# Kernel optimization log

Measured on AMD Instinct MI355X. Metric: run time of the kernel, lower is better.

The kernel has to match this reference:

```python
import jax, jax.numpy as jnp
import numpy as np

FS = 24000.0
C_SOUND = 343.0
MAX_TAU = 6
IGNORE = -100
PAIRS = np.array([(0, 1), (0, 2), (0, 3), (1, 2), (1, 3), (2, 3)])  # m1<m2 loop order
PERMS_NP = np.array([(0, 1, 2), (0, 2, 1), (1, 0, 2), (1, 2, 0), (2, 0, 1), (2, 1, 0)])  # itertools order


def _mic_locs():
    # [rad, azi_deg, ele_deg] per mic, centered at origin (matches center_mic_coords)
    coords = np.array([[0.042, 45, 35], [0.042, -45, -35], [0.042, 135, -35], [0.042, -135, 35]], dtype=np.float64)
    rad = coords[:, 0]
    azi = coords[:, 1] * 2 * np.pi / 360
    ele = coords[:, 2] * 2 * np.pi / 360
    locs = np.stack([rad * np.cos(azi) * np.cos(ele), rad * np.sin(azi) * np.cos(ele), rad * np.sin(ele)], axis=1)
    return jnp.asarray(locs, dtype=jnp.float32)

MIC_LOCS = _mic_locs()  # [4,3]


def _get_tdoa_targets(target):
    """Vectorized get_tdoa_target. target: [B,T,E,5,C].
    Assumes <=1 active class per (b,t,track) so the random class shuffle is a no-op.
    Returns (tdoas, tdoas2) as int32 [B,T,E,6]."""
    B, T, E, F, C = target.shape
    active = target[:, :, :, 0, :]                                  # [B,T,E,C] 0/1 flags
    is_active = jnp.any(active > 0, axis=-1)                        # [B,T,E]
    doa = jnp.einsum('btec,btedc->bted', active, target[:, :, :, 1:4, :])  # [B,T,E,3]
    dist = jnp.einsum('btec,btec->bte', active, target[:, :, :, 4, :])     # [B,T,E]
    src = doa * dist[..., None]                                     # [B,T,E,3]
    d = jnp.linalg.norm(src[..., None, :] - MIC_LOCS, axis=-1)      # [B,T,E,4] dist to each mic
    tdoa = d[..., PAIRS[:, 0]] - d[..., PAIRS[:, 1]]                # [B,T,E,6]
    tdoa = jnp.round(tdoa * FS / C_SOUND) + MAX_TAU                 # [B,T,E,6]
    # compact active tracks to the front (stable keeps track order, matching tr_cnt)
    order = jnp.argsort(jnp.logical_not(is_active), axis=-1)        # [B,T,E]
    gathered = jnp.take_along_axis(tdoa, order[..., None], axis=2)  # [B,T,E,6]
    n = jnp.sum(is_active, axis=-1)                                 # [B,T] number of events
    k = jnp.arange(E)[None, None, :]                                # slot index
    idx1 = jnp.clip(jnp.minimum(k, n[:, :, None] - 1), 0, E - 1)    # pad with LAST event
    idx2 = jnp.where(k < n[:, :, None], k, 0)                       # pad with FIRST event
    tdoas = jnp.take_along_axis(gathered, idx1[..., None], axis=2)
    tdoas2 = jnp.take_along_axis(gathered, idx2[..., None], axis=2)
    empty = (n == 0)[:, :, None, None]
    tdoas = jnp.where(empty, float(IGNORE), tdoas)
    tdoas2 = jnp.where(empty, float(IGNORE), tdoas2)
    return tdoas.astype(jnp.int32), tdoas2.astype(jnp.int32)


def _forward(pred, t_a, t_b):
    B, T, C, Tr, ntd = pred.shape
    N = B * T * ntd
    p = pred.transpose(0, 1, 4, 2, 3).reshape(N, C, Tr)             # [N,C,Tr]
    ta = t_a.transpose(0, 1, 3, 2).reshape(N, Tr)                   # [N,Tr]
    tb = t_b.transpose(0, 1, 3, 2).reshape(N, Tr)
    logp = jax.nn.log_softmax(p, axis=1)                            # [N,C,Tr]
    perms = jnp.asarray(PERMS_NP)                                   # [6,Tr]
    ar = jnp.arange(Tr)

    def pit(t):
        tc = jnp.clip(t, 0, C - 1)
        # L[n,i,j] = CE(pred track j, target track i); ignore_index -> 0
        L = -jnp.take_along_axis(logp, jnp.broadcast_to(tc[:, :, None], (N, Tr, Tr)), axis=1)
        L = jnp.where((t == IGNORE)[:, :, None], 0.0, L)
        pl = L[:, ar[None, :], perms].mean(axis=-1)                 # [N,6] per-perm mean loss
        pidx = jnp.argmin(pl, axis=1)                               # first min (matches torch loop)
        return jnp.take_along_axis(pl, pidx[:, None], axis=1)[:, 0], perms[pidx]

    loss1, perm1 = pit(ta)
    loss2, perm2 = pit(tb)
    use2 = loss2 < loss1                                            # torch.min keeps first on ties
    loss = jnp.where(use2, loss2, loss1)
    t_sel = jnp.where(use2[:, None], tb, ta)
    perm_sel = jnp.where(use2[:, None], perm2, perm1)

    pred_cls = jnp.argmax(p, axis=1)                                # [N,Tr]
    t_perm = jnp.take_along_axis(t_sel, perm_sel, axis=1)           # target reordered by opt perm
    valid = t_perm != IGNORE
    npred = jnp.sum(valid)
    correct = jnp.sum((pred_cls == t_perm) & valid)
    acc = jnp.where(npred > 0, correct.astype(jnp.float32) / jnp.maximum(npred, 1).astype(jnp.float32), 0.0)

    mask = loss > 0.0
    nval = jnp.sum(mask)
    lmean = jnp.where(nval > 0, jnp.sum(jnp.where(mask, loss, 0.0)) / jnp.maximum(nval, 1).astype(loss.dtype), 0.0)
    return lmean, acc


def setup_inputs() -> dict:
    key = jax.random.key(0)
    B, T, E, NCLS, NTD, CPRED = 128, 600, 3, 13, 6, 13
    k1, k2, k3, k4, k5 = jax.random.split(key, 5)
    pred = jax.random.normal(k1, (B, T, CPRED, E, NTD), dtype=jnp.float32)
    act_cls = jax.random.randint(k2, (B, T, E), 0, NCLS)
    act_flag = (jax.random.uniform(k3, (B, T, E)) < 0.5).astype(jnp.float32)
    onehot = jax.nn.one_hot(act_cls, NCLS, dtype=jnp.float32) * act_flag[..., None]  # <=1 active class/track
    doa = jax.random.normal(k4, (B, T, E, 3), dtype=jnp.float32)
    doa = doa / jnp.linalg.norm(doa, axis=-1, keepdims=True)
    dist = jax.random.uniform(k5, (B, T, E), minval=1.0, maxval=3.0, dtype=jnp.float32)
    target = jnp.concatenate([
        onehot[:, :, :, None, :],
        jnp.broadcast_to(doa[..., None], (B, T, E, 3, NCLS)),
        jnp.broadcast_to(dist[..., None, None], (B, T, E, 1, NCLS)),
    ], axis=3).astype(jnp.float32)                                  # [B,T,E,5,NCLS]
    return {"pred": pred, "target": target}


def reference(pred, target):
    t_a, t_b = _get_tdoa_targets(target)
    return _forward(pred, t_a, t_b)
```

## Files before the change

### kernel.cpp

```cpp
#include <hip/hip_runtime.h>
#include <cstdint>
#include <cstddef>

#define BT_TOTAL 76800
#define NCLS 13
#define IGN  (-100)

#define CPB   32
#define NBLK  (BT_TOTAL / CPB)
#define ITEMS (CPB * 6)
#define NF4T  (CPB * 195 / 4)
#define KT    7
#define NF4P  (CPB * 234 / 4)
#define KP    8

struct Partial { float ls; int lc; int cor; int val; };

__device__ __forceinline__ void stage16(const float4* __restrict__ g, float4* l) {
    __builtin_amdgcn_global_load_lds((const __attribute__((address_space(1))) void*)g,
                                     (__attribute__((address_space(3))) void*)l,
                                     16, 0, 0);
}

extern "C" __global__ __launch_bounds__(256)
void tdoa_fused(const float* __restrict__ pred, const float* __restrict__ target,
                Partial* __restrict__ part) {
    const int tid = threadIdx.x;
    const int cb  = blockIdx.x * CPB;

    __shared__ float4 sBuf4[NF4P];
    __shared__ uint32_t sTd[CPB * 12];
    const float* sBuf = (const float*)sBuf4;

    {
        const float4* gt = (const float4*)(target + (size_t)cb * 195);
#pragma unroll
        for (int k = 0; k < KT; k++) {
            const int i = k * 256 + tid;
            if (i < NF4T) stage16(gt + i, &sBuf4[i]);
        }
    }
    __syncthreads();

    if (tid < CPB) {
        const float* tg = sBuf + tid * 195;

        const float MX[4] = { 0.02432757455f,  0.02432757455f, -0.02432757455f, -0.02432757455f };
        const float MY[4] = { 0.02432757455f, -0.02432757455f,  0.02432757455f, -0.02432757455f };
        const float MZ[4] = { 0.02409021033f, -0.02409021033f, -0.02409021033f,  0.02409021033f };
        const int PI_[6] = {0,0,0,1,1,2};
        const int PJ_[6] = {1,2,3,2,3,3};

        int  td[3][6];
        bool ab[3];
        int  nact = 0;
#pragma unroll
        for (int e = 0; e < 3; e++) {
            float a[NCLS];
#pragma unroll
            for (int c = 0; c < NCLS; c++) a[c] = tg[e * 65 + c];
            bool ia = false;
#pragma unroll
            for (int c = 0; c < NCLS; c++) ia = ia || (a[c] > 0.0f);
            float d0 = 0.f, d1 = 0.f, d2 = 0.f, ds = 0.f;
#pragma unroll
            for (int c = 0; c < NCLS; c++) {
                d0 += a[c] * tg[e * 65 + 13 + c];
                d1 += a[c] * tg[e * 65 + 26 + c];
                d2 += a[c] * tg[e * 65 + 39 + c];
                ds += a[c] * tg[e * 65 + 52 + c];
            }
            const float sx = d0 * ds, sy = d1 * ds, sz = d2 * ds;
            float dm[4];
#pragma unroll
            for (int m = 0; m < 4; m++) {
                const float ex = sx - MX[m], ey = sy - MY[m], ez = sz - MZ[m];
                dm[m] = sqrtf(ex * ex + ey * ey + ez * ez);
            }
#pragma unroll
            for (int p = 0; p < 6; p++) {
                const float diff = dm[PI_[p]] - dm[PJ_[p]];
                td[e][p] = (int)rintf((diff * 24000.0f) / 343.0f) + 6;
            }
            ab[e] = ia;
            nact += ia ? 1 : 0;
        }

        const int o0 = ab[0] ? 0 : (ab[1] ? 1 : 2);
        const int o1 = (ab[0] && ab[1]) ? 1 : 2;
        const bool empty = (nact == 0);

#pragma unroll
        for (int p = 0; p < 6; p++) {
            const int g0 = (o0 == 0) ? td[0][p] : ((o0 == 1) ? td[1][p] : td[2][p]);
            const int g1 = (o1 == 1) ? td[1][p] : td[2][p];
            const int g2 = td[2][p];
            int ta0 = g0;
            int ta1 = (nact >= 2) ? g1 : g0;
            int ta2 = (nact == 3) ? g2 : ((nact == 2) ? g1 : g0);
            int tb0 = g0;
            int tb1 = (nact >= 2) ? g1 : g0;
            int tb2 = (nact == 3) ? g2 : g0;
            uint32_t w0 = (uint32_t)(ta0 & 0xff) | ((uint32_t)(ta1 & 0xff) << 8) | ((uint32_t)(ta2 & 0xff) << 16);
            uint32_t w1 = (uint32_t)(tb0 & 0xff) | ((uint32_t)(tb1 & 0xff) << 8) | ((uint32_t)(tb2 & 0xff) << 16);
            if (empty) { w0 = 0x009c9c9cu; w1 = 0x009c9c9cu; }
            sTd[tid * 12 + p * 2 + 0] = w0;
            sTd[tid * 12 + p * 2 + 1] = w1;
        }
    }
    __syncthreads();

    {
        const float4* gp = (const float4*)(pred + (size_t)cb * 234);
#pragma unroll
        for (int k = 0; k < KP; k++) {
            const int i = k * 256 + tid;
            if (i < NF4P) stage16(gp + i, &sBuf4[i]);
        }
    }
    __syncthreads();

    float lsum = 0.f;
    int   lcnt = 0, cor = 0, nval = 0;

    if (tid < ITEMS) {
        const int btl = tid / 6;
        const int p   = tid - btl * 6;
        const float* pp = sBuf + btl * 234 + p;

        float x[NCLS][3];
#pragma unroll
        for (int c = 0; c < NCLS; c++)
#pragma unroll
            for (int j = 0; j < 3; j++)
                x[c][j] = pp[c * 18 + j * 6];

        int   am[3];
        float lse[3];
#pragma unroll
        for (int j = 0; j < 3; j++) {
            float m = x[0][j]; int a = 0;
#pragma unroll
            for (int c = 1; c < NCLS; c++) { if (x[c][j] > m) { m = x[c][j]; a = c; } }
            float s = 0.f;
#pragma unroll
            for (int c = 0; c < NCLS; c++) s += expf(x[c][j] - m);
            am[j] = a; lse[j] = m + logf(s);
        }

        const uint32_t w0 = sTd[btl * 12 + p * 2 + 0];
        const uint32_t w1 = sTd[btl * 12 + p * 2 + 1];
        int ta[3], tb[3];
#pragma unroll
        for (int i = 0; i < 3; i++) {
            ta[i] = (int)(int8_t)(w0 >> (8 * i));
            tb[i] = (int)(int8_t)(w1 >> (8 * i));
        }

        float La[3][3], Lb[3][3];
#pragma unroll
        for (int i = 0; i < 3; i++) {
            const int  ca  = (ta[i] < 0) ? 0 : ta[i];
            const int  cb2 = (tb[i] < 0) ? 0 : tb[i];
            const bool ia  = (ta[i] == IGN);
            const bool ib  = (tb[i] == IGN);
#pragma unroll
            for (int j = 0; j < 3; j++) {
                La[i][j] = ia ? 0.f : (lse[j] - pp[ca  * 18 + j * 6]);
                Lb[i][j] = ib ? 0.f : (lse[j] - pp[cb2 * 18 + j * 6]);
            }
        }

        const int P0[6] = {0,0,1,1,2,2};
        const int P1[6] = {1,2,0,2,0,1};
        const int P2[6] = {2,1,2,0,1,0};
        float l1 = 0.f, l2 = 0.f; int i1 = 0, i2 = 0;
#pragma unroll
        for (int q = 0; q < 6; q++) {
            const float va = (La[0][P0[q]] + La[1][P1[q]] + La[2][P2[q]]) * (1.0f / 3.0f);
            const float vb = (Lb[0][P0[q]] + Lb[1][P1[q]] + Lb[2][P2[q]]) * (1.0f / 3.0f);
            if (q == 0) { l1 = va; l2 = vb; }
            else {
                if (va < l1) { l1 = va; i1 = q; }
                if (vb < l2) { l2 = vb; i2 = q; }
            }
        }

        const bool use2 = (l2 < l1);
        const float loss = use2 ? l2 : l1;
        const int  qsel = use2 ? i2 : i1;
        const int PK[6] = {36, 24, 33, 9, 18, 6};
        int pk = PK[0];
#pragma unroll
        for (int k = 1; k < 6; k++) pk = (qsel == k) ? PK[k] : pk;
        const int s0 = use2 ? tb[0] : ta[0];
        const int s1 = use2 ? tb[1] : ta[1];
        const int s2 = use2 ? tb[2] : ta[2];
#pragma unroll
        for (int i = 0; i < 3; i++) {
            const int pi = (pk >> (2 * i)) & 3;
            const int tp = (pi == 0) ? s0 : ((pi == 1) ? s1 : s2);
            const bool v = (tp != IGN);
            nval += v ? 1 : 0;
            cor  += (v && (am[i] == tp)) ? 1 : 0;
        }
        if (loss > 0.f) { lsum += loss; lcnt++; }
    }

#pragma unroll
    for (int off = 32; off > 0; off >>= 1) {
        lsum += __shfl_down(lsum, off, 64);
        lcnt += __shfl_down(lcnt, off, 64);
        cor  += __shfl_down(cor,  off, 64);
        nval += __shfl_down(nval, off, 64);
    }
    __shared__ float rf[4];
    __shared__ int   r1[4], r2[4], r3[4];
    const int wid = tid >> 6;
    if ((tid & 63) == 0) { rf[wid] = lsum; r1[wid] = lcnt; r2[wid] = cor; r3[wid] = nval; }
    __syncthreads();
    if (tid == 0) {
        Partial pt;
        pt.ls  = rf[0] + rf[1] + rf[2] + rf[3];
        pt.lc  = r1[0] + r1[1] + r1[2] + r1[3];
        pt.cor = r2[0] + r2[1] + r2[2] + r2[3];
        pt.val = r3[0] + r3[1] + r3[2] + r3[3];
        part[blockIdx.x] = pt;
    }
}

extern "C" __global__ __launch_bounds__(256)
void tdoa_final(const Partial* __restrict__ part, float* __restrict__ out) {
    const int tid = threadIdx.x;
    double ls = 0.0; int lc = 0, cor = 0, val = 0;
    for (int i = tid; i < NBLK; i += 256) {
        const Partial p = part[i];
        ls += (double)p.ls; lc += p.lc; cor += p.cor; val += p.val;
    }
#pragma unroll
    for (int off = 32; off > 0; off >>= 1) {
        ls  += __shfl_down(ls,  off, 64);
        lc  += __shfl_down(lc,  off, 64);
        cor += __shfl_down(cor, off, 64);
        val += __shfl_down(val, off, 64);
    }
    __shared__ double sd[4];
    __shared__ int    s1[4], s2[4], s3[4];
    const int wid = tid >> 6;
    if ((tid & 63) == 0) { sd[wid] = ls; s1[wid] = lc; s2[wid] = cor; s3[wid] = val; }
    __syncthreads();
    if (tid == 0) {
        const double L = sd[0] + sd[1] + sd[2] + sd[3];
        const int c1 = s1[0] + s1[1] + s1[2] + s1[3];
        const int c2 = s2[0] + s2[1] + s2[2] + s2[3];
        const int c3 = s3[0] + s3[1] + s3[2] + s3[3];
        out[0] = (c1 > 0) ? (float)(L / (double)c1) : 0.0f;
        out[1] = (c3 > 0) ? ((float)c2 / (float)c3) : 0.0f;
    }
}

extern "C" void kernel_launch(void* const* d_in, const int* in_sizes, int n_in,
                              void* d_out, int out_size, void* d_ws, size_t ws_size,
                              hipStream_t stream) {
    const float* pred   = (const float*)d_in[0];
    const float* target = (const float*)d_in[1];
    Partial* part = (Partial*)d_ws;
    float* out = (float*)d_out;
    hipLaunchKernelGGL(tdoa_fused, dim3(NBLK), dim3(256), 0, stream, pred, target, part);
    hipLaunchKernelGGL(tdoa_final, dim3(1),    dim3(256), 0, stream, part, out);
}
```

Baseline: 152.8 us.

## Parallelize TDOA target prologue across threads and overlap pred staging

The per-cell target decoding moves from 32 serial threads, each handling all three events and all six pairs, to one thread per (cell, event) for the mic distances and one thread per (cell, pair) for packing the TDOA words. Intermediate distances and activity flags pass through new shared arrays. The pred async load into LDS is now issued before the pair-packing phase, so it overlaps that compute and drops one barrier. Cells per block fall from 32 to 24 and threads per block from 256 to 192 (three waves), giving more, smaller blocks. The cost is an extra barrier and shared-memory round trip for the intermediates.

```diff
diff --git a/kernel.cpp b/kernel.cpp
--- a/kernel.cpp
+++ b/kernel.cpp
@@ -6,7 +6,8 @@
 #define NCLS 13
 #define IGN  (-100)
 
-#define CPB   32
+#define CPB   24
+#define BLKT  192
 #define NBLK  (BT_TOTAL / CPB)
 #define ITEMS (CPB * 6)
 #define NF4T  (CPB * 195 / 4)
@@ -22,7 +23,7 @@
                                      16, 0, 0);
 }
 
-extern "C" __global__ __launch_bounds__(256)
+extern "C" __global__ __launch_bounds__(BLKT)
 void tdoa_fused(const float* __restrict__ pred, const float* __restrict__ target,
                 Partial* __restrict__ part) {
     const int tid = threadIdx.x;
@@ -30,93 +31,97 @@
 
     __shared__ float4 sBuf4[NF4P];
     __shared__ uint32_t sTd[CPB * 12];
+    __shared__ float  dmS[CPB * 12];
+    __shared__ int    actS[CPB * 3];
     const float* sBuf = (const float*)sBuf4;
 
     {
         const float4* gt = (const float4*)(target + (size_t)cb * 195);
 #pragma unroll
         for (int k = 0; k < KT; k++) {
-            const int i = k * 256 + tid;
+            const int i = k * BLKT + tid;
             if (i < NF4T) stage16(gt + i, &sBuf4[i]);
         }
     }
     __syncthreads();
 
-    if (tid < CPB) {
-        const float* tg = sBuf + tid * 195;
+    if (tid < CPB * 3) {
+        const int cell = tid / 3;
+        const int e    = tid - cell * 3;
+        const float* tg = sBuf + cell * 195 + e * 65;
 
         const float MX[4] = { 0.02432757455f,  0.02432757455f, -0.02432757455f, -0.02432757455f };
         const float MY[4] = { 0.02432757455f, -0.02432757455f,  0.02432757455f, -0.02432757455f };
         const float MZ[4] = { 0.02409021033f, -0.02409021033f, -0.02409021033f,  0.02409021033f };
+
+        float a[NCLS];
+#pragma unroll
+        for (int c = 0; c < NCLS; c++) a[c] = tg[c];
+        bool ia = false;
+#pragma unroll
+        for (int c = 0; c < NCLS; c++) ia = ia || (a[c] > 0.0f);
+        float d0 = 0.f, d1 = 0.f, d2 = 0.f, ds = 0.f;
+#pragma unroll
+        for (int c = 0; c < NCLS; c++) {
+            d0 += a[c] * tg[13 + c];
+            d1 += a[c] * tg[26 + c];
+            d2 += a[c] * tg[39 + c];
+            ds += a[c] * tg[52 + c];
+        }
+        const float sx = d0 * ds, sy = d1 * ds, sz = d2 * ds;
+#pragma unroll
+        for (int m = 0; m < 4; m++) {
+            const float ex = sx - MX[m], ey = sy - MY[m], ez = sz - MZ[m];
+            dmS[cell * 12 + e * 4 + m] = sqrtf(ex * ex + ey * ey + ez * ez);
+        }
+        actS[cell * 3 + e] = ia ? 1 : 0;
+    }
+    __syncthreads();
+
+    {
+        const float4* gp = (const float4*)(pred + (size_t)cb * 234);
+#pragma unroll
+        for (int k = 0; k < KP; k++) {
+            const int i = k * BLKT + tid;
+            if (i < NF4P) stage16(gp + i, &sBuf4[i]);
+        }
+    }
+
+    if (tid < ITEMS) {
+        const int cell = tid / 6;
+        const int p    = tid - cell * 6;
         const int PI_[6] = {0,0,0,1,1,2};
         const int PJ_[6] = {1,2,3,2,3,3};
-
-        int  td[3][6];
-        bool ab[3];
-        int  nact = 0;
+        const int mi = PI_[p], mj = PJ_[p];
+
+        int td[3];
 #pragma unroll
         for (int e = 0; e < 3; e++) {
-            float a[NCLS];
-#pragma unroll
-            for (int c = 0; c < NCLS; c++) a[c] = tg[e * 65 + c];
-            bool ia = false;
-#pragma unroll
-            for (int c = 0; c < NCLS; c++) ia = ia || (a[c] > 0.0f);
-            float d0 = 0.f, d1 = 0.f, d2 = 0.f, ds = 0.f;
-#pragma unroll
-            for (int c = 0; c < NCLS; c++) {
-                d0 += a[c] * tg[e * 65 + 13 + c];
-                d1 += a[c] * tg[e * 65 + 26 + c];
-                d2 += a[c] * tg[e * 65 + 39 + c];
-                ds += a[c] * tg[e * 65 + 52 + c];
-            }
-            const float sx = d0 * ds, sy = d1 * ds, sz = d2 * ds;
-            float dm[4];
-#pragma unroll
-            for (int m = 0; m < 4; m++) {
-                const float ex = sx - MX[m], ey = sy - MY[m], ez = sz - MZ[m];
-                dm[m] = sqrtf(ex * ex + ey * ey + ez * ez);
-            }
-#pragma unroll
-            for (int p = 0; p < 6; p++) {
-                const float diff = dm[PI_[p]] - dm[PJ_[p]];
-                td[e][p] = (int)rintf((diff * 24000.0f) / 343.0f) + 6;
-            }
-            ab[e] = ia;
-            nact += ia ? 1 : 0;
-        }
-
-        const int o0 = ab[0] ? 0 : (ab[1] ? 1 : 2);
-        const int o1 = (ab[0] && ab[1]) ? 1 : 2;
-        const bool empty = (nact == 0);
-
-#pragma unroll
-        for (int p = 0; p < 6; p++) {
-            const int g0 = (o0 == 0) ? td[0][p] : ((o0 == 1) ? td[1][p] : td[2][p]);
-            const int g1 = (o1 == 1) ? td[1][p] : td[2][p];
-            const int g2 = td[2][p];
-            int ta0 = g0;
-            int ta1 = (nact >= 2) ? g1 : g0;
-            int ta2 = (nact == 3) ? g2 : ((nact == 2) ? g1 : g0);
-            int tb0 = g0;
-            int tb1 = (nact >= 2) ? g1 : g0;
-            int tb2 = (nact == 3) ? g2 : g0;
-            uint32_t w0 = (uint32_t)(ta0 & 0xff) | ((uint32_t)(ta1 & 0xff) << 8) | ((uint32_t)(ta2 & 0xff) << 16);
-            uint32_t w1 = (uint32_t)(tb0 & 0xff) | ((uint32_t)(tb1 & 0xff) << 8) | ((uint32_t)(tb2 & 0xff) << 16);
-            if (empty) { w0 = 0x009c9c9cu; w1 = 0x009c9c9cu; }
-            sTd[tid * 12 + p * 2 + 0] = w0;
-            sTd[tid * 12 + p * 2 + 1] = w1;
-        }
-    }
-    __syncthreads();
-
-    {
-        const float4* gp = (const float4*)(pred + (size_t)cb * 234);
-#pragma unroll
-        for (int k = 0; k < KP; k++) {
-            const int i = k * 256 + tid;
-            if (i < NF4P) stage16(gp + i, &sBuf4[i]);
-        }
+            const float diff = dmS[cell * 12 + e * 4 + mi] - dmS[cell * 12 + e * 4 + mj];
+            td[e] = (int)rintf((diff * 24000.0f) / 343.0f) + 6;
+        }
+        const bool ab0 = actS[cell * 3 + 0] != 0;
+        const bool ab1 = actS[cell * 3 + 1] != 0;
+        const bool ab2 = actS[cell * 3 + 2] != 0;
+        const int  nact = (ab0 ? 1 : 0) + (ab1 ? 1 : 0) + (ab2 ? 1 : 0);
+
+        const int o0 = ab0 ? 0 : (ab1 ? 1 : 2);
+        const int o1 = (ab0 && ab1) ? 1 : 2;
+
+        const int g0 = (o0 == 0) ? td[0] : ((o0 == 1) ? td[1] : td[2]);
+        const int g1 = (o1 == 1) ? td[1] : td[2];
+        const int g2 = td[2];
+        int ta0 = g0;
+        int ta1 = (nact >= 2) ? g1 : g0;
+        int ta2 = (nact == 3) ? g2 : ((nact == 2) ? g1 : g0);
+        int tb0 = g0;
+        int tb1 = (nact >= 2) ? g1 : g0;
+        int tb2 = (nact == 3) ? g2 : g0;
+        uint32_t w0 = (uint32_t)(ta0 & 0xff) | ((uint32_t)(ta1 & 0xff) << 8) | ((uint32_t)(ta2 & 0xff) << 16);
+        uint32_t w1 = (uint32_t)(tb0 & 0xff) | ((uint32_t)(tb1 & 0xff) << 8) | ((uint32_t)(tb2 & 0xff) << 16);
+        if (nact == 0) { w0 = 0x009c9c9cu; w1 = 0x009c9c9cu; }
+        sTd[cell * 12 + p * 2 + 0] = w0;
+        sTd[cell * 12 + p * 2 + 1] = w1;
     }
     __syncthreads();
 
@@ -214,17 +219,17 @@
         cor  += __shfl_down(cor,  off, 64);
         nval += __shfl_down(nval, off, 64);
     }
-    __shared__ float rf[4];
-    __shared__ int   r1[4], r2[4], r3[4];
+    __shared__ float rf[3];
+    __shared__ int   r1[3], r2[3], r3[3];
     const int wid = tid >> 6;
     if ((tid & 63) == 0) { rf[wid] = lsum; r1[wid] = lcnt; r2[wid] = cor; r3[wid] = nval; }
     __syncthreads();
     if (tid == 0) {
         Partial pt;
-        pt.ls  = rf[0] + rf[1] + rf[2] + rf[3];
-        pt.lc  = r1[0] + r1[1] + r1[2] + r1[3];
-        pt.cor = r2[0] + r2[1] + r2[2] + r2[3];
-        pt.val = r3[0] + r3[1] + r3[2] + r3[3];
+        pt.ls  = rf[0] + rf[1] + rf[2];
+        pt.lc  = r1[0] + r1[1] + r1[2];
+        pt.cor = r2[0] + r2[1] + r2[2];
+        pt.val = r3[0] + r3[1] + r3[2];
         part[blockIdx.x] = pt;
     }
 }
@@ -266,6 +271,6 @@
     const float* target = (const float*)d_in[1];
     Partial* part = (Partial*)d_ws;
     float* out = (float*)d_out;
-    hipLaunchKernelGGL(tdoa_fused, dim3(NBLK), dim3(256), 0, stream, pred, target, part);
-    hipLaunchKernelGGL(tdoa_final, dim3(1),    dim3(256), 0, stream, part, out);
-}
+    hipLaunchKernelGGL(tdoa_fused, dim3(NBLK), dim3(BLKT), 0, stream, pred, target, part);
+    hipLaunchKernelGGL(tdoa_final, dim3(1),    dim3(256),  0, stream, part, out);
+}
```

Result: slower. 156.5 us (+2.5%).
